# Kernel optimization log

Hardware: AMD Instinct MI355X
Metric: run time of the kernel (lower is better)

The kernel has to match this reference:

```python
import jax, jax.numpy as jnp
import numpy as np

B, T, H = 8, 2048, 1024
P = 64           # num_attention_project
N = 4096         # config.n (bias table length), N >= 2T-1
WINDOW = 64      # relative_attention
NEG = -10000.0


def setup_inputs() -> dict:
    key = jax.random.key(0)
    ks = jax.random.split(key, 10)
    s = 1.0 / np.sqrt(H)
    sp = 1.0 / np.sqrt(P)
    sb = 1.0 / np.sqrt(N)
    return {
        "attn_input": jax.random.normal(ks[0], (B, T, H), dtype=jnp.float32),
        "attention_mask": jnp.ones((B, T), dtype=jnp.float32),
        # Linear weights stored as [in, out] so y = x @ W + b
        "Wq": jax.random.uniform(ks[1], (H, P), minval=-s, maxval=s),
        "bq": jnp.zeros((P,), jnp.float32),
        "Wk": jax.random.uniform(ks[2], (H, P), minval=-s, maxval=s),
        "bk": jnp.zeros((P,), jnp.float32),
        "Wv": jax.random.uniform(ks[3], (H, P), minval=-s, maxval=s),
        "bv": jnp.zeros((P,), jnp.float32),
        "Wo": jax.random.uniform(ks[4], (P, H), minval=-sp, maxval=sp),
        "bo": jnp.zeros((H,), jnp.float32),
        "bias": jax.random.uniform(ks[5], (N,), minval=-sb, maxval=sb),
    }


def reference(attn_input, attention_mask, Wq, bq, Wk, bk, Wv, bv, Wo, bo, bias):
    q = attn_input @ Wq + bq            # [B,T,P]
    k = attn_input @ Wk + bk
    v = attn_input @ Wv + bv
    scores = jnp.einsum("btp,bsp->bts", q, k) / jnp.sqrt(jnp.float32(P))  # [B,T,T]
    # padding mask: note original broadcasts over COLUMNS via unsqueeze(-1)
    scores = scores + (1.0 - attention_mask)[:, :, None] * NEG
    # circulant window mask: keep |i-j| <= WINDOW (all ones if WINDOW >= T)
    i = jnp.arange(T)
    rel = i[:, None] - i[None, :]       # i - j
    win = (jnp.abs(rel) <= WINDOW) | (WINDOW >= T)
    scores = scores + jnp.where(win, 0.0, NEG)[None, :, :]
    # gathered learnable relative-position bias: bias[n//2 - i + j]
    scores = scores + bias[N // 2 - rel][None, :, :]
    attn = jax.nn.softmax(scores, axis=-1)
    out = jnp.einsum("bts,bsp->btp", attn, v)
    return out @ Wo + bo                # [B,T,H]
```

## Files before the change

### kernel.cpp

```cpp
#include <hip/hip_runtime.h>

using bf16x8 = __attribute__((ext_vector_type(8))) short;
using f32x4  = __attribute__((ext_vector_type(4))) float;

static __device__ inline unsigned short f2bf(float f) {
  unsigned int u = __float_as_uint(f);
  u += 0x7fffu + ((u >> 16) & 1u);
  return (unsigned short)(u >> 16);
}
static __device__ inline unsigned int pk2(float a, float b) {
  return (unsigned int)f2bf(a) | ((unsigned int)f2bf(b) << 16);
}

#define ROW16_MAX(x) { \
  { int _t = __builtin_amdgcn_update_dpp(0, __float_as_int(x), 0x121, 0xf, 0xf, true); x = fmaxf(x, __int_as_float(_t)); } \
  { int _t = __builtin_amdgcn_update_dpp(0, __float_as_int(x), 0x122, 0xf, 0xf, true); x = fmaxf(x, __int_as_float(_t)); } \
  { int _t = __builtin_amdgcn_update_dpp(0, __float_as_int(x), 0x124, 0xf, 0xf, true); x = fmaxf(x, __int_as_float(_t)); } \
  { int _t = __builtin_amdgcn_update_dpp(0, __float_as_int(x), 0x128, 0xf, 0xf, true); x = fmaxf(x, __int_as_float(_t)); } }
#define ROW16_SUM(x) { \
  { int _t = __builtin_amdgcn_update_dpp(0, __float_as_int(x), 0x121, 0xf, 0xf, true); x += __int_as_float(_t); } \
  { int _t = __builtin_amdgcn_update_dpp(0, __float_as_int(x), 0x122, 0xf, 0xf, true); x += __int_as_float(_t); } \
  { int _t = __builtin_amdgcn_update_dpp(0, __float_as_int(x), 0x124, 0xf, 0xf, true); x += __int_as_float(_t); } \
  { int _t = __builtin_amdgcn_update_dpp(0, __float_as_int(x), 0x128, 0xf, 0xf, true); x += __int_as_float(_t); } }

__global__ __launch_bounds__(256) void prep_kernel(
    const float* __restrict__ Wq, const float* __restrict__ Wk, const float* __restrict__ Wv,
    const float* __restrict__ Wo, const float* __restrict__ bq, const float* __restrict__ bk,
    const float* __restrict__ bv,
    unsigned short* __restrict__ Wt, unsigned short* __restrict__ Wot, float* __restrict__ bqkv)
{
  int idx = blockIdx.x * 256 + threadIdx.x;
  if (idx < 192 * 1024) {
    int n = idx >> 10, k = idx & 1023;
    const float* W = (n < 64) ? Wq : (n < 128) ? Wk : Wv;
    Wt[idx] = f2bf(W[k * 64 + (n & 63)]);
  } else if (idx < 192 * 1024 + 1024 * 64) {
    int j = idx - 192 * 1024;
    int n = j >> 6, k = j & 63;
    Wot[j] = f2bf(Wo[k * 1024 + n]);
  } else if (idx < 192 * 1024 + 1024 * 64 + 192) {
    int n = idx - (192 * 1024 + 1024 * 64);
    bqkv[n] = (n < 64) ? bq[n] : (n < 128) ? bk[n - 64] : bv[n - 128];
  }
}

__global__ __launch_bounds__(256) void qkv_gemm(
    const float* __restrict__ X, const unsigned short* __restrict__ Wt,
    const float* __restrict__ bqkv, float* __restrict__ qkv)
{
  __shared__ __align__(16) unsigned short As[32 * 72];
  __shared__ __align__(16) unsigned short Bs[192 * 72];
  int t = threadIdx.x;
  int lane = t & 63, w = t >> 6;
  int m0 = blockIdx.x * 32;
  int mg = w & 1, ng = w >> 1;
  int col = lane & 15, quad = lane >> 4;
  f32x4 acc[6] = {};

  for (int ks = 0; ks < 16; ++ks) {
    __syncthreads();
    {
      int row = t >> 3, c = t & 7;
      const float* src = X + (size_t)(m0 + row) * 1024 + ks * 64 + c * 8;
      float4 f0 = *(const float4*)(src);
      float4 f1 = *(const float4*)(src + 4);
      uint4 p;
      p.x = pk2(f0.x, f0.y); p.y = pk2(f0.z, f0.w);
      p.z = pk2(f1.x, f1.y); p.w = pk2(f1.z, f1.w);
      *(uint4*)(As + row * 72 + c * 8) = p;
    }
    #pragma unroll
    for (int r = 0; r < 6; ++r) {
      int tau = t + 256 * r;
      int n = tau >> 3, c = tau & 7;
      *(uint4*)(Bs + n * 72 + c * 8) =
          *(const uint4*)(Wt + (size_t)n * 1024 + ks * 64 + c * 8);
    }
    __syncthreads();
    #pragma unroll
    for (int kk = 0; kk < 64; kk += 32) {
      int ko = kk + quad * 8;
      bf16x8 a = *(const bf16x8*)(As + (mg * 16 + col) * 72 + ko);
      #pragma unroll
      for (int ns = 0; ns < 6; ++ns) {
        bf16x8 b = *(const bf16x8*)(Bs + ((ng * 6 + ns) * 16 + col) * 72 + ko);
        acc[ns] = __builtin_amdgcn_mfma_f32_16x16x32_bf16(a, b, acc[ns], 0, 0, 0);
      }
    }
  }
  #pragma unroll
  for (int ns = 0; ns < 6; ++ns)
    #pragma unroll
    for (int r = 0; r < 4; ++r) {
      int m = m0 + mg * 16 + quad * 4 + r;
      int n = ng * 96 + ns * 16 + col;
      qkv[(size_t)m * 192 + n] = acc[ns][r] + bqkv[n];
    }
}

__global__ __launch_bounds__(256) void band_attn(
    const float* __restrict__ qkv, const float* __restrict__ bias,
    unsigned short* __restrict__ attnout)
{
  __shared__ __align__(16) unsigned short Kl[192 * 72];
  __shared__ __align__(16) unsigned short Vt[64 * 216];
  __shared__ __align__(16) unsigned short Ps[4 * 16 * 168];
  __shared__ float biasL[129];

  int t = threadIdx.x;
  int lane = t & 63, w = t >> 6;
  int col = lane & 15, quad = lane >> 4;
  int bidx = blockIdx.x;
  int b = bidx >> 5;
  int i0 = (bidx & 31) * 64;
  int jw = i0 - 64;
  const float* qbase = qkv + (size_t)(b << 11) * 192;

  if (t < 129) biasL[t] = bias[1984 + t];
  #pragma unroll
  for (int it = 0; it < 24; ++it) {
    int row = it * 8 + (t >> 5);
    int colq = (t & 31) * 4;
    int jb = jw + row;
    int jc = jb < 0 ? 0 : (jb > 2047 ? 2047 : jb);
    const float* src = qbase + (size_t)jc * 192 + 64 + colq;
    float4 f = *(const float4*)src;
    if (colq < 64) {
      *(uint2*)(Kl + row * 72 + colq) = make_uint2(pk2(f.x, f.y), pk2(f.z, f.w));
    } else {
      int p0 = colq - 64;
      Vt[(p0 + 0) * 216 + row] = f2bf(f.x);
      Vt[(p0 + 1) * 216 + row] = f2bf(f.y);
      Vt[(p0 + 2) * 216 + row] = f2bf(f.z);
      Vt[(p0 + 3) * 216 + row] = f2bf(f.w);
    }
  }
  {
    int p = t >> 2, c0 = 192 + (t & 3) * 4;
    *(uint2*)(Vt + p * 216 + c0) = make_uint2(0u, 0u);
  }
  __syncthreads();

  int iq = i0 + w * 16;
  bf16x8 aq0, aq1;
  {
    const float* qr = qbase + (size_t)(iq + col) * 192 + quad * 8;
    float4 f0 = *(const float4*)(qr);
    float4 f1 = *(const float4*)(qr + 4);
    float4 f2 = *(const float4*)(qr + 32);
    float4 f3 = *(const float4*)(qr + 36);
    union { bf16x8 v; uint4 u; } c0_, c1_;
    c0_.u = make_uint4(pk2(f0.x, f0.y), pk2(f0.z, f0.w), pk2(f1.x, f1.y), pk2(f1.z, f1.w));
    c1_.u = make_uint4(pk2(f2.x, f2.y), pk2(f2.z, f2.w), pk2(f3.x, f3.y), pk2(f3.z, f3.w));
    aq0 = c0_.v; aq1 = c1_.v;
  }
  f32x4 s[9];
  #pragma unroll
  for (int t9 = 0; t9 < 9; ++t9) {
    int krow = ((w + t9) * 16 + col) * 72;
    bf16x8 kb0 = *(const bf16x8*)(Kl + krow + quad * 8);
    bf16x8 kb1 = *(const bf16x8*)(Kl + krow + 32 + quad * 8);
    f32x4 z = {};
    z = __builtin_amdgcn_mfma_f32_16x16x32_bf16(aq0, kb0, z, 0, 0, 0);
    s[t9] = __builtin_amdgcn_mfma_f32_16x16x32_bf16(aq1, kb1, z, 0, 0, 0);
  }
  int q4 = quad * 4;
  float mrow[4] = {-3e38f, -3e38f, -3e38f, -3e38f};
  #pragma unroll
  for (int t9 = 0; t9 < 9; ++t9) {
    int j = iq - 64 + t9 * 16 + col;
    #pragma unroll
    for (int r = 0; r < 4; ++r) {
      int diff = q4 + r + 64 - t9 * 16 - col;
      bool valid = (j >= 0) & (j < 2048) & (diff >= -64) & (diff <= 64);
      int bi = 64 - diff; bi = bi < 0 ? 0 : (bi > 128 ? 128 : bi);
      float sv = valid ? (s[t9][r] * 0.125f + biasL[bi]) : -3e38f;
      s[t9][r] = sv;
      mrow[r] = fmaxf(mrow[r], sv);
    }
  }
  #pragma unroll
  for (int r = 0; r < 4; ++r) ROW16_MAX(mrow[r]);
  unsigned short* Pw = Ps + w * (16 * 168);
  float lsum[4] = {0.f, 0.f, 0.f, 0.f};
  #pragma unroll
  for (int t9 = 0; t9 < 9; ++t9)
    #pragma unroll
    for (int r = 0; r < 4; ++r) {
      float p = __expf(s[t9][r] - mrow[r]);
      lsum[r] += p;
      Pw[(q4 + r) * 168 + t9 * 16 + col] = f2bf(p);
    }
  #pragma unroll
  for (int r = 0; r < 4; ++r) {
    ROW16_SUM(lsum[r]);
    Pw[(q4 + r) * 168 + 144 + col] = 0;
  }
  f32x4 o[4] = {};
  #pragma unroll
  for (int kc = 0; kc < 5; ++kc) {
    bf16x8 pa = *(const bf16x8*)(Pw + col * 168 + kc * 32 + quad * 8);
    #pragma unroll
    for (int nt = 0; nt < 4; ++nt) {
      bf16x8 vb = *(const bf16x8*)(Vt + (nt * 16 + col) * 216 + 16 * w + kc * 32 + quad * 8);
      o[nt] = __builtin_amdgcn_mfma_f32_16x16x32_bf16(pa, vb, o[nt], 0, 0, 0);
    }
  }
  float rl[4];
  #pragma unroll
  for (int r = 0; r < 4; ++r) rl[r] = 1.0f / lsum[r];
  #pragma unroll
  for (int nt = 0; nt < 4; ++nt)
    #pragma unroll
    for (int r = 0; r < 4; ++r) {
      int arow = (b << 11) + iq + q4 + r;
      attnout[(size_t)arow * 64 + nt * 16 + col] = f2bf(o[nt][r] * rl[r]);
    }
}

__global__ __launch_bounds__(256) void out_gemm(
    const unsigned short* __restrict__ attn, const unsigned short* __restrict__ Wot,
    const float* __restrict__ bo, float* __restrict__ out)
{
  __shared__ __align__(16) unsigned short As[64 * 72];
  __shared__ __align__(16) unsigned short Bs[128 * 72];
  int t = threadIdx.x, lane = t & 63, w = t >> 6;
  int m0 = (blockIdx.x >> 3) * 64;
  int n0 = (blockIdx.x & 7) * 128;
  #pragma unroll
  for (int r = 0; r < 2; ++r) {
    int tau = t + 256 * r; int row = tau >> 3, c = tau & 7;
    *(uint4*)(As + row * 72 + c * 8) =
        *(const uint4*)(attn + (size_t)(m0 + row) * 64 + c * 8);
  }
  #pragma unroll
  for (int r = 0; r < 4; ++r) {
    int tau = t + 256 * r; int n = tau >> 3, c = tau & 7;
    *(uint4*)(Bs + n * 72 + c * 8) =
        *(const uint4*)(Wot + (size_t)(n0 + n) * 64 + c * 8);
  }
  __syncthreads();
  f32x4 acc[2][4] = {};
  int mg = w & 1, ngg = w >> 1;
  #pragma unroll
  for (int kk = 0; kk < 64; kk += 32) {
    int ko = kk + (lane >> 4) * 8;
    bf16x8 a0 = *(const bf16x8*)(As + (mg * 32 +      (lane & 15)) * 72 + ko);
    bf16x8 a1 = *(const bf16x8*)(As + (mg * 32 + 16 + (lane & 15)) * 72 + ko);
    #pragma unroll
    for (int ns = 0; ns < 4; ++ns) {
      bf16x8 b = *(const bf16x8*)(Bs + ((ngg * 4 + ns) * 16 + (lane & 15)) * 72 + ko);
      acc[0][ns] = __builtin_amdgcn_mfma_f32_16x16x32_bf16(a0, b, acc[0][ns], 0, 0, 0);
      acc[1][ns] = __builtin_amdgcn_mfma_f32_16x16x32_bf16(a1, b, acc[1][ns], 0, 0, 0);
    }
  }
  int col = lane & 15, q = lane >> 4;
  #pragma unroll
  for (int ms = 0; ms < 2; ++ms)
    #pragma unroll
    for (int ns = 0; ns < 4; ++ns)
      #pragma unroll
      for (int r = 0; r < 4; ++r) {
        int mm = m0 + mg * 32 + ms * 16 + q * 4 + r;
        int nn = n0 + (ngg * 4 + ns) * 16 + col;
        out[(size_t)mm * 1024 + nn] = acc[ms][ns][r] + bo[nn];
      }
}

extern "C" void kernel_launch(void* const* d_in, const int* in_sizes, int n_in,
                              void* d_out, int out_size, void* d_ws, size_t ws_size,
                              hipStream_t stream) {
  const float* X    = (const float*)d_in[0];
  const float* Wq   = (const float*)d_in[2];
  const float* bq   = (const float*)d_in[3];
  const float* Wk   = (const float*)d_in[4];
  const float* bk   = (const float*)d_in[5];
  const float* Wv   = (const float*)d_in[6];
  const float* bv   = (const float*)d_in[7];
  const float* Wo   = (const float*)d_in[8];
  const float* bo   = (const float*)d_in[9];
  const float* bias = (const float*)d_in[10];
  float* out = (float*)d_out;
  char* ws = (char*)d_ws;
  float*          qkv  = (float*)(ws);
  unsigned short* attn = (unsigned short*)(ws + 12582912);
  unsigned short* Wt   = (unsigned short*)(ws + 14680064);
  unsigned short* Wot  = (unsigned short*)(ws + 15073280);
  float*          bqkv = (float*)(ws + 15204352);

  prep_kernel<<<1025, 256, 0, stream>>>(Wq, Wk, Wv, Wo, bq, bk, bv, Wt, Wot, bqkv);
  qkv_gemm<<<512, 256, 0, stream>>>(X, Wt, bqkv, qkv);
  band_attn<<<256, 256, 0, stream>>>(qkv, bias, attn);
  out_gemm<<<2048, 256, 0, stream>>>(attn, Wot, bo, out);
}
```

Baseline: 185.9 us.

## Double-buffer QKV GEMM shared tiles with register prefetch of next K-slice

Converts the QKV projection GEMM to use two LDS buffers. The next K-slice of X and the weights is loaded into registers before the MFMA loop and written to the other buffer afterwards, removing one barrier per iteration. The goal is to hide global-load latency behind the matrix math. It doubles LDS use and raises register pressure, which may lower occupancy.

Result: slower. 210.0 us (+12.9%).

```diff
diff --git a/kernel.cpp b/kernel.cpp
--- a/kernel.cpp
+++ b/kernel.cpp
@@ -48,8 +48,8 @@
     const float* __restrict__ X, const unsigned short* __restrict__ Wt,
     const float* __restrict__ bqkv, float* __restrict__ qkv)
 {
-  __shared__ __align__(16) unsigned short As[32 * 72];
-  __shared__ __align__(16) unsigned short Bs[192 * 72];
+  __shared__ __align__(16) unsigned short As[2][32 * 72];
+  __shared__ __align__(16) unsigned short Bs[2][192 * 72];
   int t = threadIdx.x;
   int lane = t & 63, w = t >> 6;
   int m0 = blockIdx.x * 32;
@@ -57,35 +57,57 @@
   int col = lane & 15, quad = lane >> 4;
   f32x4 acc[6] = {};
 
+  int rowA = t >> 3, cA = t & 7;
+  int nB = t >> 3, cB = t & 7;
+  const float* srcA = X + (size_t)(m0 + rowA) * 1024 + cA * 8;
+  const unsigned short* srcB = Wt + (size_t)nB * 1024 + cB * 8;
+
+  float4 a0, a1; uint4 breg[6];
+  a0 = *(const float4*)(srcA);
+  a1 = *(const float4*)(srcA + 4);
+  #pragma unroll
+  for (int r = 0; r < 6; ++r)
+    breg[r] = *(const uint4*)(srcB + (size_t)r * 32 * 1024);
+  {
+    uint4 p; p.x = pk2(a0.x, a0.y); p.y = pk2(a0.z, a0.w);
+    p.z = pk2(a1.x, a1.y); p.w = pk2(a1.z, a1.w);
+    *(uint4*)(&As[0][rowA * 72 + cA * 8]) = p;
+    #pragma unroll
+    for (int r = 0; r < 6; ++r)
+      *(uint4*)(&Bs[0][(nB + 32 * r) * 72 + cB * 8]) = breg[r];
+  }
+
+  #pragma unroll 2
   for (int ks = 0; ks < 16; ++ks) {
-    __syncthreads();
-    {
-      int row = t >> 3, c = t & 7;
-      const float* src = X + (size_t)(m0 + row) * 1024 + ks * 64 + c * 8;
-      float4 f0 = *(const float4*)(src);
-      float4 f1 = *(const float4*)(src + 4);
-      uint4 p;
-      p.x = pk2(f0.x, f0.y); p.y = pk2(f0.z, f0.w);
-      p.z = pk2(f1.x, f1.y); p.w = pk2(f1.z, f1.w);
-      *(uint4*)(As + row * 72 + c * 8) = p;
-    }
-    #pragma unroll
-    for (int r = 0; r < 6; ++r) {
-      int tau = t + 256 * r;
-      int n = tau >> 3, c = tau & 7;
-      *(uint4*)(Bs + n * 72 + c * 8) =
-          *(const uint4*)(Wt + (size_t)n * 1024 + ks * 64 + c * 8);
+    int cur = ks & 1;
+    float4 na0, na1; uint4 nb[6];
+    if (ks < 15) {
+      const float* sA = srcA + (ks + 1) * 64;
+      na0 = *(const float4*)(sA);
+      na1 = *(const float4*)(sA + 4);
+      const unsigned short* sB = srcB + (ks + 1) * 64;
+      #pragma unroll
+      for (int r = 0; r < 6; ++r)
+        nb[r] = *(const uint4*)(sB + (size_t)r * 32 * 1024);
     }
     __syncthreads();
     #pragma unroll
     for (int kk = 0; kk < 64; kk += 32) {
       int ko = kk + quad * 8;
-      bf16x8 a = *(const bf16x8*)(As + (mg * 16 + col) * 72 + ko);
+      bf16x8 a = *(const bf16x8*)(&As[cur][(mg * 16 + col) * 72 + ko]);
       #pragma unroll
       for (int ns = 0; ns < 6; ++ns) {
-        bf16x8 b = *(const bf16x8*)(Bs + ((ng * 6 + ns) * 16 + col) * 72 + ko);
+        bf16x8 b = *(const bf16x8*)(&Bs[cur][((ng * 6 + ns) * 16 + col) * 72 + ko]);
         acc[ns] = __builtin_amdgcn_mfma_f32_16x16x32_bf16(a, b, acc[ns], 0, 0, 0);
       }
+    }
+    if (ks < 15) {
+      uint4 p; p.x = pk2(na0.x, na0.y); p.y = pk2(na0.z, na0.w);
+      p.z = pk2(na1.x, na1.y); p.w = pk2(na1.z, na1.w);
+      *(uint4*)(&As[cur ^ 1][rowA * 72 + cA * 8]) = p;
+      #pragma unroll
+      for (int r = 0; r < 6; ++r)
+        *(uint4*)(&Bs[cur ^ 1][(nB + 32 * r) * 72 + cB * 8]) = nb[r];
     }
   }
   #pragma unroll
```
